# Kernel tuning notes

Measured on AMD Instinct MI355X. Metric: run time of the kernel, lower is better.

## Reference

```python
import jax, jax.numpy as jnp
import numpy as np

B, M, N, Z = 4, 64, 64, 64
IN_DIM, OUT_DIM = 32, 32
MODES1 = MODES2 = MODES3 = 16
HIDDEN = OUT_DIM * 4  # factor=4, n_ff_layers=2
LN_EPS = 1e-5


def setup_inputs() -> dict:
    key = jax.random.key(0)
    ks = jax.random.split(key, 10)
    # xavier-normal-ish scale for (in, out, modes, 2) fourier weights
    fscale = np.sqrt(2.0 / (IN_DIM + OUT_DIM))
    x = jax.random.normal(ks[0], (B, M, N, Z, IN_DIM), dtype=jnp.float32)
    wx = jax.random.normal(ks[1], (IN_DIM, OUT_DIM, MODES1, 2), dtype=jnp.float32) * fscale
    wy = jax.random.normal(ks[2], (IN_DIM, OUT_DIM, MODES2, 2), dtype=jnp.float32) * fscale
    wz = jax.random.normal(ks[3], (IN_DIM, OUT_DIM, MODES3, 2), dtype=jnp.float32) * fscale
    # FeedForward: Linear(OUT_DIM, HIDDEN) + ReLU, then Linear(HIDDEN, OUT_DIM) + LayerNorm
    w0 = jax.random.normal(ks[4], (OUT_DIM, HIDDEN), dtype=jnp.float32) * np.sqrt(1.0 / OUT_DIM)
    b0 = jnp.zeros((HIDDEN,), dtype=jnp.float32)
    w1 = jax.random.normal(ks[5], (HIDDEN, OUT_DIM), dtype=jnp.float32) * np.sqrt(1.0 / HIDDEN)
    b1 = jnp.zeros((OUT_DIM,), dtype=jnp.float32)
    ln_g = jnp.ones((OUT_DIM,), dtype=jnp.float32)
    ln_b = jnp.zeros((OUT_DIM,), dtype=jnp.float32)
    return {"x": x, "wx": wx, "wy": wy, "wz": wz,
            "w0": w0, "b0": b0, "w1": w1, "b1": b1,
            "ln_g": ln_g, "ln_b": ln_b}


def _as_complex(w):
    return w[..., 0] + 1j * w[..., 1]


def _forward_fourier(x, wx, wy, wz):
    # x: [b, m, n, z, i] -> [b, i, m, n, z]
    xt = jnp.transpose(x, (0, 4, 1, 2, 3))
    # --- axis M (dim 2) ---
    ftx = jnp.fft.rfft(xt, axis=2, norm='ortho')  # [b, i, M//2+1, n, z] complex
    ox = jnp.einsum('bixyz,iox->boxyz', ftx[:, :, :MODES1], _as_complex(wx))
    ox = jnp.pad(ox, ((0, 0), (0, 0), (0, M // 2 + 1 - MODES1), (0, 0), (0, 0)))
    xx = jnp.fft.irfft(ox, n=M, axis=2, norm='ortho')
    # --- axis N (dim 3) ---
    fty = jnp.fft.rfft(xt, axis=3, norm='ortho')
    oy = jnp.einsum('bixyz,ioy->boxyz', fty[:, :, :, :MODES2], _as_complex(wy))
    oy = jnp.pad(oy, ((0, 0), (0, 0), (0, 0), (0, N // 2 + 1 - MODES2), (0, 0)))
    xy = jnp.fft.irfft(oy, n=N, axis=3, norm='ortho')
    # --- axis Z (dim 4) ---
    ftz = jnp.fft.rfft(xt, axis=4, norm='ortho')
    oz = jnp.einsum('bixyz,ioz->boxyz', ftz[:, :, :, :, :MODES3], _as_complex(wz))
    oz = jnp.pad(oz, ((0, 0), (0, 0), (0, 0), (0, 0), (0, Z // 2 + 1 - MODES3)))
    xz = jnp.fft.irfft(oz, n=Z, axis=4, norm='ortho')
    out = xx + xy + xz  # [b, o, m, n, z]
    return jnp.transpose(out, (0, 2, 3, 4, 1))  # [b, m, n, z, o]


def reference(x, wx, wy, wz, w0, b0, w1, b1, ln_g, ln_b):
    s = _forward_fourier(x, wx, wy, wz)
    h = jax.nn.relu(s @ w0 + b0)
    y = h @ w1 + b1
    mu = jnp.mean(y, axis=-1, keepdims=True)
    var = jnp.mean((y - mu) ** 2, axis=-1, keepdims=True)
    y = (y - mu) * jax.lax.rsqrt(var + LN_EPS) * ln_g + ln_b
    return y
```

## Files before the change

### kernel.cpp

```cpp
#include <hip/hip_runtime.h>
#include <math.h>

typedef __attribute__((ext_vector_type(8))) short short8v;
typedef __attribute__((ext_vector_type(4))) float float4v;

constexpr float THETA = 6.28318530717958647692f / 64.0f;

constexpr int S_B = 64 * 64 * 64 * 32;
constexpr int S_M = 64 * 64 * 32;
constexpr int S_N = 64 * 32;
constexpr int S_Z = 32;

__device__ __forceinline__ unsigned short f2bf(float f) {
    __bf16 h = (__bf16)f;
    return __builtin_bit_cast(unsigned short, h);
}
__device__ __forceinline__ unsigned int pkbf(float lo, float hi) {
    return (unsigned int)f2bf(lo) | ((unsigned int)f2bf(hi) << 16);
}
__device__ __forceinline__ float bf2f(unsigned int h) {
    return __builtin_bit_cast(float, h << 16);
}

constexpr int WS_TF = 98304, WS_TI = 100352, WS_TOTAL = 102400;

__global__ __launch_bounds__(256)
void setup_frags(const float* __restrict__ wx, const float* __restrict__ wy,
                 const float* __restrict__ wz, unsigned short* __restrict__ W)
{
    int f0 = (blockIdx.x * 256 + threadIdx.x) * 4;
#pragma unroll
    for (int u = 0; u < 4; ++u) {
        int f = f0 + u;
        if (f >= WS_TOTAL) continue;
        unsigned short v;
        if (f < WS_TF) {
            int ax = f >> 15, rem = f & 32767;
            int k = rem >> 11;
            int rem2 = rem & 2047;
            int wt = rem2 >> 10, rt = (rem2 >> 9) & 1, l = (rem2 >> 3) & 63, e = rem2 & 7;
            int o = 16 * rt + (l & 15), i = 8 * (l >> 4) + e;
            const float* w = (ax == 0) ? wx : ((ax == 1) ? wy : wz);
            v = f2bf(w[((i * 32 + o) * 16 + k) * 2 + wt]);
        } else if (f < WS_TI) {
            int rem = f - WS_TF;
            int jt = rem >> 10, s = (rem >> 9) & 1, l = (rem >> 3) & 63, e = rem & 7;
            int kk = l & 15, m = 32 * s + 8 * (l >> 4) + e;
            int jm = (kk * m) & 63;
            float ang = THETA * (float)jm;
            v = f2bf(jt == 0 ? cosf(ang) : sinf(ang));
        } else {
            int rem = f - WS_TI;
            int mt = rem >> 9, l = (rem >> 3) & 63, e = rem & 7;
            int mp = 16 * mt + (l & 15), r = 8 * (l >> 4) + e;
            int k = r & 15;
            float sk = (k == 0) ? (1.0f / 64.0f) : (2.0f / 64.0f);
            int jm = (k * mp) & 63;
            float ang = THETA * (float)jm;
            v = f2bf(r < 16 ? sk * cosf(ang) : -sk * sinf(ang));
        }
        W[f] = v;
    }
}

constexpr int AB_SHORTS = 4096;
__device__ __forceinline__ int ab4(int t, int k, int line, int i) {
    return ((((t * 16 + k) * 4 + line) * 64) + i * 2) ^ (((line ^ k) & 7) << 4);
}
constexpr int P_LS = 1288;
constexpr int P_SHORTS = 4 * P_LS;
__device__ __forceinline__ int p4(int line, int o, int r) {
    return line * P_LS + o * 40 + r;
}

template <int STRIDE>
__device__ __forceinline__ void stageF1(const float* __restrict__ x, long bs,
                                        const unsigned short* __restrict__ tf,
                                        unsigned short* __restrict__ AB,
                                        int lane, int line)
{
    const int gq = lane >> 4, c = lane & 15;
    short8v tfB[2][2];
#pragma unroll
    for (int jt = 0; jt < 2; ++jt)
#pragma unroll
        for (int s = 0; s < 2; ++s)
            tfB[jt][s] = *reinterpret_cast<const short8v*>(tf + ((jt * 2 + s) * 64 + lane) * 8);

    float xr[2][2][8];
#pragma unroll
    for (int rt = 0; rt < 2; ++rt) {
        const float* xp = x + bs + 16 * rt + c;
#pragma unroll
        for (int s = 0; s < 2; ++s)
#pragma unroll
            for (int e = 0; e < 8; ++e)
                xr[rt][s][e] = xp[(long)(32 * s + 8 * gq + e) * STRIDE];
    }

    float4v acc[2][2];
#pragma unroll
    for (int rt = 0; rt < 2; ++rt)
#pragma unroll
        for (int jt = 0; jt < 2; ++jt)
            acc[rt][jt] = float4v{0.f, 0.f, 0.f, 0.f};

#pragma unroll
    for (int rt = 0; rt < 2; ++rt)
#pragma unroll
        for (int s = 0; s < 2; ++s) {
            short8v a;
#pragma unroll
            for (int e = 0; e < 8; ++e)
                a[e] = (short)f2bf(xr[rt][s][e]);
            acc[rt][0] = __builtin_amdgcn_mfma_f32_16x16x32_bf16(a, tfB[0][s], acc[rt][0], 0, 0, 0);
            acc[rt][1] = __builtin_amdgcn_mfma_f32_16x16x32_bf16(a, tfB[1][s], acc[rt][1], 0, 0, 0);
        }

#pragma unroll
    for (int rt = 0; rt < 2; ++rt)
#pragma unroll
        for (int jt = 0; jt < 2; ++jt) {
            *reinterpret_cast<uint2*>(reinterpret_cast<char*>(AB) + ab4(jt, c, line, 16 * rt + 4 * gq)) =
                make_uint2(pkbf(acc[rt][jt][0], acc[rt][jt][1]), pkbf(acc[rt][jt][2], acc[rt][jt][3]));
        }
}

__device__ __forceinline__ void stageMx4(const unsigned short* __restrict__ wf,
                                         const unsigned short* __restrict__ AB,
                                         unsigned short* __restrict__ P,
                                         int lane, int wave)
{
    const int gq = lane >> 4, c = lane & 15;
    const int t2 = wave >> 1, rt = wave & 1, lc = c & 3;
    for (int k = 0; k < 16; k += 2) {
        float4v acc2[2];
#pragma unroll
        for (int kk = 0; kk < 2; ++kk) {
            const int kc = k + kk;
            short8v aT = *reinterpret_cast<const short8v*>(reinterpret_cast<const char*>(AB) + ab4(0, kc, lc, 8 * gq));
            short8v bT = *reinterpret_cast<const short8v*>(reinterpret_cast<const char*>(AB) + ab4(1, kc, lc, 8 * gq));
            const int w1t = t2 ? 1 : 0, w2t = t2 ? 0 : 1;
            short8v w1 = *reinterpret_cast<const short8v*>(wf + (((kc * 2 + w1t) * 2 + rt) * 64 + lane) * 8);
            short8v w2 = *reinterpret_cast<const short8v*>(wf + (((kc * 2 + w2t) * 2 + rt) * 64 + lane) * 8);
            if (t2) {
                union { short8v s; unsigned int u[4]; } nb;
                nb.s = bT;
#pragma unroll
                for (int j = 0; j < 4; ++j) nb.u[j] ^= 0x80008000u;
                bT = nb.s;
            }
            float4v a2 = float4v{0.f, 0.f, 0.f, 0.f};
            a2 = __builtin_amdgcn_mfma_f32_16x16x32_bf16(w1, aT, a2, 0, 0, 0);
            a2 = __builtin_amdgcn_mfma_f32_16x16x32_bf16(w2, bT, a2, 0, 0, 0);
            acc2[kk] = a2;
        }
        if (c < 4) {
#pragma unroll
            for (int r = 0; r < 4; ++r) {
                *reinterpret_cast<unsigned int*>(&P[p4(c, 16 * rt + 4 * gq + r, 16 * t2 + k)]) =
                    pkbf(acc2[0][r], acc2[1][r]);
            }
        }
    }
}

template <int AXIS, int MODE>
__global__ __launch_bounds__(256, 4)
void spectral_mfma(const float* __restrict__ x,
                   const unsigned short* __restrict__ wf,
                   const unsigned short* __restrict__ tf,
                   const unsigned short* __restrict__ ti,
                   float* __restrict__ out,
                   unsigned short* __restrict__ pw)
{
    __shared__ __align__(16) unsigned short AB[AB_SHORTS];
    __shared__ __align__(16) unsigned short P[P_SHORTS];

    const int t = threadIdx.x, lane = t & 63, wave = t >> 6;
    const int gq = lane >> 4, c = lane & 15;
    constexpr int stride = (AXIS == 0) ? S_M : S_N;

    const int l = blockIdx.x * 4 + wave;
    const int b = l >> 12, p1 = (l >> 6) & 63, p2 = l & 63;
    const long bs = (AXIS == 0)
        ? (long)b * S_B + (long)p1 * S_N + (long)p2 * S_Z
        : (long)b * S_B + (long)p1 * S_M + (long)p2 * S_Z;

    stageF1<stride>(x, bs, tf, AB, lane, wave);
    __syncthreads();
    stageMx4(wf, AB, P, lane, wave);
    __syncthreads();

    short8v tiB[4];
#pragma unroll
    for (int mt = 0; mt < 4; ++mt)
        tiB[mt] = *reinterpret_cast<const short8v*>(ti + (mt * 64 + lane) * 8);

    short8v pA[2];
    pA[0] = *reinterpret_cast<const short8v*>(&P[p4(wave, c, 8 * gq)]);
    pA[1] = *reinterpret_cast<const short8v*>(&P[p4(wave, 16 + c, 8 * gq)]);

#pragma unroll
    for (int rt = 0; rt < 2; ++rt)
#pragma unroll
        for (int mt = 0; mt < 4; ++mt) {
            float4v acc = float4v{0.f, 0.f, 0.f, 0.f};
            acc = __builtin_amdgcn_mfma_f32_16x16x32_bf16(pA[rt], tiB[mt], acc, 0, 0, 0);
            const long off = bs + (long)(16 * mt + c) * stride + 16 * rt + 4 * gq;
            if (MODE == 0) {
                *reinterpret_cast<float4*>(out + off) = make_float4(acc[0], acc[1], acc[2], acc[3]);
            } else if (MODE == 1) {
                float4 old = *reinterpret_cast<const float4*>(out + off);
                old.x += acc[0]; old.y += acc[1]; old.z += acc[2]; old.w += acc[3];
                *reinterpret_cast<float4*>(out + off) = old;
            } else if (MODE == 2) {
                *reinterpret_cast<uint2*>(pw + off) =
                    make_uint2(pkbf(acc[0], acc[1]), pkbf(acc[2], acc[3]));
            } else {
                uint2 old = *reinterpret_cast<const uint2*>(pw + off);
                const float v0 = bf2f(old.x & 0xffffu) + acc[0];
                const float v1 = bf2f(old.x >> 16)     + acc[1];
                const float v2 = bf2f(old.y & 0xffffu) + acc[2];
                const float v3 = bf2f(old.y >> 16)     + acc[3];
                *reinterpret_cast<uint2*>(pw + off) =
                    make_uint2(pkbf(v0, v1), pkbf(v2, v3));
            }
        }
}

template <int NPART>
__global__ __launch_bounds__(256)
void spectral_fused(const float* __restrict__ x,
                    const unsigned short* __restrict__ wf,
                    const unsigned short* __restrict__ tf,
                    const unsigned short* __restrict__ ti,
                    const float* __restrict__ w0, const float* __restrict__ b0,
                    const float* __restrict__ w1, const float* __restrict__ b1,
                    const float* __restrict__ g,  const float* __restrict__ bb,
                    const unsigned short* __restrict__ pw1,
                    const unsigned short* __restrict__ pw2,
                    const float* __restrict__ pf32,
                    float* __restrict__ out)
{
    __shared__ __align__(16) unsigned short sm[23584];
    constexpr int OP = 8192, OS = 13344;

    const int t = threadIdx.x, lane = t & 63, wave = t >> 6;
    const int gq = lane >> 4, c = lane & 15;

    const int l = blockIdx.x * 4 + wave;
    const int b = l >> 12, p1 = (l >> 6) & 63, p2 = l & 63;
    const long bs = (long)b * S_B + (long)p1 * S_M + (long)p2 * S_N;

    float4 b0q[8];
#pragma unroll
    for (int n = 0; n < 8; ++n)
        b0q[n] = *reinterpret_cast<const float4*>(b0 + 16 * n + 4 * gq);
    float b1v[2], gv[2], bvv[2];
#pragma unroll
    for (int n = 0; n < 2; ++n) { b1v[n] = b1[n * 16 + c]; gv[n] = g[n * 16 + c]; bvv[n] = bb[n * 16 + c]; }

    stageF1<S_Z>(x, bs, tf, sm, lane, wave);
    __syncthreads();
    stageMx4(wf, sm, sm + OP, lane, wave);
    __syncthreads();

    for (int s = t; s < 512; s += 256) {
        const int n = s >> 6, ln = s & 63, g2 = ln >> 4, c2 = ln & 15;
        const int kb = n >> 1, nn = n & 1;
        short8v v0, v1;
#pragma unroll
        for (int e = 0; e < 8; ++e) {
            v0[e] = (short)f2bf(w0[(8 * g2 + e) * 128 + n * 16 + c2]);
            v1[e] = (short)f2bf(w1[(32 * kb + 8 * g2 + e) * 32 + nn * 16 + c2]);
        }
        *reinterpret_cast<short8v*>(&sm[s * 8])        = v0;
        *reinterpret_cast<short8v*>(&sm[4096 + s * 8]) = v1;
    }

    short8v tiB[4];
#pragma unroll
    for (int mt = 0; mt < 4; ++mt)
        tiB[mt] = *reinterpret_cast<const short8v*>(ti + (mt * 64 + lane) * 8);

    {
        short8v pA[2];
        pA[0] = *reinterpret_cast<const short8v*>(&sm[OP + p4(wave, c, 8 * gq)]);
        pA[1] = *reinterpret_cast<const short8v*>(&sm[OP + p4(wave, 16 + c, 8 * gq)]);
#pragma unroll
        for (int rt = 0; rt < 2; ++rt)
#pragma unroll
            for (int mt = 0; mt < 4; ++mt) {
                float4v acc = float4v{0.f, 0.f, 0.f, 0.f};
                acc = __builtin_amdgcn_mfma_f32_16x16x32_bf16(pA[rt], tiB[mt], acc, 0, 0, 0);
                const long off = bs + (long)(16 * mt + c) * S_Z + 16 * rt + 4 * gq;
                float v0, v1, v2, v3;
                if (NPART == 0) {
                    float4 old = *reinterpret_cast<const float4*>(pf32 + off);
                    v0 = old.x + acc[0]; v1 = old.y + acc[1];
                    v2 = old.z + acc[2]; v3 = old.w + acc[3];
                } else {
                    uint2 pv = *reinterpret_cast<const uint2*>(pw1 + off);
                    v0 = bf2f(pv.x & 0xffffu) + acc[0];
                    v1 = bf2f(pv.x >> 16)     + acc[1];
                    v2 = bf2f(pv.y & 0xffffu) + acc[2];
                    v3 = bf2f(pv.y >> 16)     + acc[3];
                    if (NPART == 2) {
                        uint2 qv = *reinterpret_cast<const uint2*>(pw2 + off);
                        v0 += bf2f(qv.x & 0xffffu);
                        v1 += bf2f(qv.x >> 16);
                        v2 += bf2f(qv.y & 0xffffu);
                        v3 += bf2f(qv.y >> 16);
                    }
                }
                const int si = OS + (wave * 64 + 16 * mt + c) * 40 + 16 * rt + 4 * gq;
                *reinterpret_cast<uint2*>(&sm[si]) = make_uint2(pkbf(v0, v1), pkbf(v2, v3));
            }
    }
    __syncthreads();

    const int Hb = OS + wave * 2560;

    short8v af[4];
#pragma unroll
    for (int f = 0; f < 4; ++f)
        af[f] = *reinterpret_cast<const short8v*>(&sm[OS + (wave * 64 + 16 * f + c) * 40 + 8 * gq]);

    float4v Y[4][2];
#pragma unroll
    for (int f = 0; f < 4; ++f)
#pragma unroll
        for (int n = 0; n < 2; ++n)
            Y[f][n] = float4v{b1v[n], b1v[n], b1v[n], b1v[n]};

#pragma unroll
    for (int kb = 0; kb < 4; ++kb) {
#pragma unroll
        for (int nn = 0; nn < 2; ++nn) {
            const int n = 2 * kb + nn;
            const short8v wv = *reinterpret_cast<const short8v*>(&sm[(n * 64 + lane) * 8]);
#pragma unroll
            for (int f = 0; f < 4; ++f) {
                float4v hacc = float4v{b0q[n].x, b0q[n].y, b0q[n].z, b0q[n].w};
                hacc = __builtin_amdgcn_mfma_f32_16x16x32_bf16(wv, af[f], hacc, 0, 0, 0);
                const float h0 = fmaxf(hacc[0], 0.f), h1 = fmaxf(hacc[1], 0.f);
                const float h2 = fmaxf(hacc[2], 0.f), h3 = fmaxf(hacc[3], 0.f);
                *reinterpret_cast<uint2*>(&sm[Hb + (16 * f + c) * 40 + 16 * nn + 4 * gq]) =
                    make_uint2(pkbf(h0, h1), pkbf(h2, h3));
            }
        }
        const short8v wva = *reinterpret_cast<const short8v*>(&sm[4096 + ((kb * 2 + 0) * 64 + lane) * 8]);
        const short8v wvb = *reinterpret_cast<const short8v*>(&sm[4096 + ((kb * 2 + 1) * 64 + lane) * 8]);
#pragma unroll
        for (int f = 0; f < 4; ++f) {
            const short8v a2 = *reinterpret_cast<const short8v*>(&sm[Hb + (16 * f + c) * 40 + 8 * gq]);
            Y[f][0] = __builtin_amdgcn_mfma_f32_16x16x32_bf16(a2, wva, Y[f][0], 0, 0, 0);
            Y[f][1] = __builtin_amdgcn_mfma_f32_16x16x32_bf16(a2, wvb, Y[f][1], 0, 0, 0);
        }
    }

#pragma unroll
    for (int f = 0; f < 4; ++f) {
        float smv[4], sq[4];
#pragma unroll
        for (int r = 0; r < 4; ++r) {
            const float v0 = Y[f][0][r], v1 = Y[f][1][r];
            smv[r] = v0 + v1;
            sq[r]  = v0 * v0 + v1 * v1;
        }
#pragma unroll
        for (int mask = 1; mask <= 8; mask <<= 1) {
#pragma unroll
            for (int r = 0; r < 4; ++r) {
                smv[r] += __shfl_xor(smv[r], mask);
                sq[r]  += __shfl_xor(sq[r], mask);
            }
        }
#pragma unroll
        for (int r = 0; r < 4; ++r) {
            const float mu = smv[r] * (1.0f / 32.0f);
            const float var = sq[r] * (1.0f / 32.0f) - mu * mu;
            const float rs = rsqrtf(var + 1e-5f);
            float* op = out + bs + (long)(16 * f + 4 * gq + r) * 32;
            op[c]      = (Y[f][0][r] - mu) * rs * gv[0] + bvv[0];
            op[16 + c] = (Y[f][1][r] - mu) * rs * gv[1] + bvv[1];
        }
    }
}

extern "C" void kernel_launch(void* const* d_in, const int* in_sizes, int n_in,
                              void* d_out, int out_size, void* d_ws, size_t ws_size,
                              hipStream_t stream)
{
    const float* x    = (const float*)d_in[0];
    const float* wx   = (const float*)d_in[1];
    const float* wy   = (const float*)d_in[2];
    const float* wz   = (const float*)d_in[3];
    const float* w0   = (const float*)d_in[4];
    const float* b0   = (const float*)d_in[5];
    const float* w1   = (const float*)d_in[6];
    const float* b1   = (const float*)d_in[7];
    const float* ln_g = (const float*)d_in[8];
    const float* ln_b = (const float*)d_in[9];
    float* out = (float*)d_out;

    unsigned short* wsf = (unsigned short*)d_ws;

    const size_t PART_OFF   = 262144;
    const size_t PART_BYTES = (size_t)33554432 * 2;
    unsigned short* pw1 = (unsigned short*)((char*)d_ws + PART_OFF);
    unsigned short* pw2 = (unsigned short*)((char*)d_ws + PART_OFF + PART_BYTES);
    const int tier = (ws_size >= PART_OFF + 2 * PART_BYTES) ? 2
                   : (ws_size >= PART_OFF + PART_BYTES)     ? 1 : 0;

    setup_frags<<<100, 256, 0, stream>>>(wx, wy, wz, wsf);

    if (tier == 2) {
        spectral_mfma<0, 2><<<4096, 256, 0, stream>>>(x, wsf + 0 * 32768, wsf + WS_TF, wsf + WS_TI, out, pw1);
        spectral_mfma<1, 2><<<4096, 256, 0, stream>>>(x, wsf + 1 * 32768, wsf + WS_TF, wsf + WS_TI, out, pw2);
        spectral_fused<2><<<4096, 256, 0, stream>>>(x, wsf + 2 * 32768, wsf + WS_TF, wsf + WS_TI,
                                                    w0, b0, w1, b1, ln_g, ln_b, pw1, pw2, out, out);
    } else if (tier == 1) {
        spectral_mfma<0, 2><<<4096, 256, 0, stream>>>(x, wsf + 0 * 32768, wsf + WS_TF, wsf + WS_TI, out, pw1);
        spectral_mfma<1, 3><<<4096, 256, 0, stream>>>(x, wsf + 1 * 32768, wsf + WS_TF, wsf + WS_TI, out, pw1);
        spectral_fused<1><<<4096, 256, 0, stream>>>(x, wsf + 2 * 32768, wsf + WS_TF, wsf + WS_TI,
                                                    w0, b0, w1, b1, ln_g, ln_b, pw1, pw1, out, out);
    } else {
        spectral_mfma<0, 0><<<4096, 256, 0, stream>>>(x, wsf + 0 * 32768, wsf + WS_TF, wsf + WS_TI, out, pw1);
        spectral_mfma<1, 1><<<4096, 256, 0, stream>>>(x, wsf + 1 * 32768, wsf + WS_TF, wsf + WS_TI, out, pw1);
        spectral_fused<0><<<4096, 256, 0, stream>>>(x, wsf + 2 * 32768, wsf + WS_TF, wsf + WS_TI,
                                                    w0, b0, w1, b1, ln_g, ln_b, pw1, pw1, out, out);
    }
}
```

Baseline: 234.4 us.

## Alias spectral P buffer with FFN scratch to cut LDS and relax launch bounds

The final Z-axis kernel now puts each wave's spectral P region in the same per-wave slice later reused for the summed activations and hidden tiles. An XOR swizzle on that region avoids bank conflicts, and the change shrinks shared memory from about 47KB to 37KB so more blocks can be resident. The first stage now converts x loads directly into MFMA operands instead of buffering them all in registers first. The min-blocks hint is dropped from the spectral kernels. The aliasing relies on the existing barriers keeping the P reads ahead of the overwrites, and interleaving loads with MFMAs may expose more memory latency.

```diff
diff --git a/kernel.cpp b/kernel.cpp
--- a/kernel.cpp
+++ b/kernel.cpp
@@ -69,9 +69,6 @@
 }
 constexpr int P_LS = 1288;
 constexpr int P_SHORTS = 4 * P_LS;
-__device__ __forceinline__ int p4(int line, int o, int r) {
-    return line * P_LS + o * 40 + r;
-}
 
 template <int STRIDE>
 __device__ __forceinline__ void stageF1(const float* __restrict__ x, long bs,
@@ -87,36 +84,26 @@
         for (int s = 0; s < 2; ++s)
             tfB[jt][s] = *reinterpret_cast<const short8v*>(tf + ((jt * 2 + s) * 64 + lane) * 8);
 
-    float xr[2][2][8];
+    float4v acc[2][2];
+#pragma unroll
+    for (int rt = 0; rt < 2; ++rt)
+#pragma unroll
+        for (int jt = 0; jt < 2; ++jt)
+            acc[rt][jt] = float4v{0.f, 0.f, 0.f, 0.f};
+
 #pragma unroll
     for (int rt = 0; rt < 2; ++rt) {
         const float* xp = x + bs + 16 * rt + c;
 #pragma unroll
-        for (int s = 0; s < 2; ++s)
-#pragma unroll
-            for (int e = 0; e < 8; ++e)
-                xr[rt][s][e] = xp[(long)(32 * s + 8 * gq + e) * STRIDE];
-    }
-
-    float4v acc[2][2];
-#pragma unroll
-    for (int rt = 0; rt < 2; ++rt)
-#pragma unroll
-        for (int jt = 0; jt < 2; ++jt)
-            acc[rt][jt] = float4v{0.f, 0.f, 0.f, 0.f};
-
-#pragma unroll
-    for (int rt = 0; rt < 2; ++rt)
-#pragma unroll
         for (int s = 0; s < 2; ++s) {
             short8v a;
 #pragma unroll
             for (int e = 0; e < 8; ++e)
-                a[e] = (short)f2bf(xr[rt][s][e]);
+                a[e] = (short)f2bf(xp[(long)(32 * s + 8 * gq + e) * STRIDE]);
             acc[rt][0] = __builtin_amdgcn_mfma_f32_16x16x32_bf16(a, tfB[0][s], acc[rt][0], 0, 0, 0);
             acc[rt][1] = __builtin_amdgcn_mfma_f32_16x16x32_bf16(a, tfB[1][s], acc[rt][1], 0, 0, 0);
         }
-
+    }
 #pragma unroll
     for (int rt = 0; rt < 2; ++rt)
 #pragma unroll
@@ -126,6 +113,7 @@
         }
 }
 
+template <int PITCH, bool XS>
 __device__ __forceinline__ void stageMx4(const unsigned short* __restrict__ wf,
                                          const unsigned short* __restrict__ AB,
                                          unsigned short* __restrict__ P,
@@ -158,7 +146,9 @@
         if (c < 4) {
 #pragma unroll
             for (int r = 0; r < 4; ++r) {
-                *reinterpret_cast<unsigned int*>(&P[p4(c, 16 * rt + 4 * gq + r, 16 * t2 + k)]) =
+                int inner = (16 * rt + 4 * gq + r) * 40 + 16 * t2 + k;
+                if (XS) inner ^= (c << 3);
+                *reinterpret_cast<unsigned int*>(&P[c * PITCH + inner]) =
                     pkbf(acc2[0][r], acc2[1][r]);
             }
         }
@@ -166,7 +156,7 @@
 }
 
 template <int AXIS, int MODE>
-__global__ __launch_bounds__(256, 4)
+__global__ __launch_bounds__(256)
 void spectral_mfma(const float* __restrict__ x,
                    const unsigned short* __restrict__ wf,
                    const unsigned short* __restrict__ tf,
@@ -189,7 +179,7 @@
 
     stageF1<stride>(x, bs, tf, AB, lane, wave);
     __syncthreads();
-    stageMx4(wf, AB, P, lane, wave);
+    stageMx4<P_LS, false>(wf, AB, P, lane, wave);
     __syncthreads();
 
     short8v tiB[4];
@@ -198,8 +188,8 @@
         tiB[mt] = *reinterpret_cast<const short8v*>(ti + (mt * 64 + lane) * 8);
 
     short8v pA[2];
-    pA[0] = *reinterpret_cast<const short8v*>(&P[p4(wave, c, 8 * gq)]);
-    pA[1] = *reinterpret_cast<const short8v*>(&P[p4(wave, 16 + c, 8 * gq)]);
+    pA[0] = *reinterpret_cast<const short8v*>(&P[wave * P_LS + c * 40 + 8 * gq]);
+    pA[1] = *reinterpret_cast<const short8v*>(&P[wave * P_LS + (16 + c) * 40 + 8 * gq]);
 
 #pragma unroll
     for (int rt = 0; rt < 2; ++rt)
@@ -243,11 +233,12 @@
                     const float* __restrict__ pf32,
                     float* __restrict__ out)
 {
-    __shared__ __align__(16) unsigned short sm[23584];
-    constexpr int OP = 8192, OS = 13344;
+    __shared__ __align__(16) unsigned short sm[18432];
+    constexpr int OP = 8192;
 
     const int t = threadIdx.x, lane = t & 63, wave = t >> 6;
     const int gq = lane >> 4, c = lane & 15;
+    const int SB = OP + wave * 2560;
 
     const int l = blockIdx.x * 4 + wave;
     const int b = l >> 12, p1 = (l >> 6) & 63, p2 = l & 63;
@@ -263,7 +254,7 @@
 
     stageF1<S_Z>(x, bs, tf, sm, lane, wave);
     __syncthreads();
-    stageMx4(wf, sm, sm + OP, lane, wave);
+    stageMx4<2560, true>(wf, sm, sm + OP, lane, wave);
     __syncthreads();
 
     for (int s = t; s < 512; s += 256) {
@@ -286,8 +277,8 @@
 
     {
         short8v pA[2];
-        pA[0] = *reinterpret_cast<const short8v*>(&sm[OP + p4(wave, c, 8 * gq)]);
-        pA[1] = *reinterpret_cast<const short8v*>(&sm[OP + p4(wave, 16 + c, 8 * gq)]);
+        pA[0] = *reinterpret_cast<const short8v*>(&sm[SB + ((c * 40 + 8 * gq) ^ (wave << 3))]);
+        pA[1] = *reinterpret_cast<const short8v*>(&sm[SB + (((16 + c) * 40 + 8 * gq) ^ (wave << 3))]);
 #pragma unroll
         for (int rt = 0; rt < 2; ++rt)
 #pragma unroll
@@ -314,18 +305,16 @@
                         v3 += bf2f(qv.y >> 16);
                     }
                 }
-                const int si = OS + (wave * 64 + 16 * mt + c) * 40 + 16 * rt + 4 * gq;
+                const int si = SB + (16 * mt + c) * 40 + 16 * rt + 4 * gq;
                 *reinterpret_cast<uint2*>(&sm[si]) = make_uint2(pkbf(v0, v1), pkbf(v2, v3));
             }
     }
     __syncthreads();
 
-    const int Hb = OS + wave * 2560;
-
     short8v af[4];
 #pragma unroll
     for (int f = 0; f < 4; ++f)
-        af[f] = *reinterpret_cast<const short8v*>(&sm[OS + (wave * 64 + 16 * f + c) * 40 + 8 * gq]);
+        af[f] = *reinterpret_cast<const short8v*>(&sm[SB + (16 * f + c) * 40 + 8 * gq]);
 
     float4v Y[4][2];
 #pragma unroll
@@ -346,7 +335,7 @@
                 hacc = __builtin_amdgcn_mfma_f32_16x16x32_bf16(wv, af[f], hacc, 0, 0, 0);
                 const float h0 = fmaxf(hacc[0], 0.f), h1 = fmaxf(hacc[1], 0.f);
                 const float h2 = fmaxf(hacc[2], 0.f), h3 = fmaxf(hacc[3], 0.f);
-                *reinterpret_cast<uint2*>(&sm[Hb + (16 * f + c) * 40 + 16 * nn + 4 * gq]) =
+                *reinterpret_cast<uint2*>(&sm[SB + (16 * f + c) * 40 + 16 * nn + 4 * gq]) =
                     make_uint2(pkbf(h0, h1), pkbf(h2, h3));
             }
         }
@@ -354,7 +343,7 @@
         const short8v wvb = *reinterpret_cast<const short8v*>(&sm[4096 + ((kb * 2 + 1) * 64 + lane) * 8]);
 #pragma unroll
         for (int f = 0; f < 4; ++f) {
-            const short8v a2 = *reinterpret_cast<const short8v*>(&sm[Hb + (16 * f + c) * 40 + 8 * gq]);
+            const short8v a2 = *reinterpret_cast<const short8v*>(&sm[SB + (16 * f + c) * 40 + 8 * gq]);
             Y[f][0] = __builtin_amdgcn_mfma_f32_16x16x32_bf16(a2, wva, Y[f][0], 0, 0, 0);
             Y[f][1] = __builtin_amdgcn_mfma_f32_16x16x32_bf16(a2, wvb, Y[f][1], 0, 0, 0);
         }
```

Result: slower. 248.1 us (+5.9%).
